# Kernel tuning notes

Measured on AMD Instinct MI355X. Metric: run time of the kernel, lower is better.

The kernel has to match this reference:

```python
import jax, jax.numpy as jnp
import numpy as np

B, T, D, TY = 64, 512, 96, 512
H, DK = 4, 32            # num_heads, embed_dim_per_head
E = H * DK               # embed_dim = 128
P = 2                    # function='L' -> 2 coefficients
L, HID = 64, 128         # latent_dim, hidden_dim


def setup_inputs() -> dict:
    key = jax.random.key(0)
    ks = jax.random.split(key, 16)
    inp = {
        "timesteps": jax.random.uniform(ks[0], (B, T), jnp.float32),
        "X": jax.random.normal(ks[1], (B, T, D), jnp.float32),
        "M": jax.random.randint(ks[2], (B, T, D), 0, 2).astype(jnp.float32),
        "y_time_steps": jax.random.uniform(ks[3], (B, TY), jnp.float32),
        # time_embedding: Linear(1, E)
        "te_w": jax.random.normal(ks[4], (E,), jnp.float32),
        "te_b": jax.random.normal(ks[5], (E,), jnp.float32) * 0.1,
        # learned query [1, P, E]
        "query": jax.random.normal(ks[6], (1, P, E), jnp.float32),
        # query_map / key_map: Linear(E, E), stored [in, out]
        "q_w": jax.random.normal(ks[7], (E, E), jnp.float32) / np.sqrt(E),
        "q_b": jax.random.normal(ks[8], (E,), jnp.float32) * 0.1,
        "k_w": jax.random.normal(ks[9], (E, E), jnp.float32) / np.sqrt(E),
        "k_b": jax.random.normal(ks[10], (E,), jnp.float32) * 0.1,
        # attn shared out: Linear(2D*H, L)
        "ow": jax.random.normal(ks[11], (2 * D * H, L), jnp.float32) / np.sqrt(2 * D * H),
        "ob": jnp.zeros((L,), jnp.float32),
        # decoder MLP: Linear(L,HID)+ReLU+Linear(HID,D)
        "w1": jax.random.normal(ks[12], (L, HID), jnp.float32) / np.sqrt(L),
        "b1": jnp.zeros((HID,), jnp.float32),
        "w2": jax.random.normal(ks[13], (HID, D), jnp.float32) / np.sqrt(HID),
        "b2": jnp.zeros((D,), jnp.float32),
    }
    return inp


def _fld_forward(timesteps, X, M, y_time_steps, te_w, te_b, query,
                 q_w, q_b, k_w, k_b, ow, ob, w1, b1, w2, b2):
    b, t, d = X.shape
    # time embedding: Linear(1,E), sin applied to indices i % H == 0
    emb = timesteps[..., None] * te_w + te_b               # [B,T,E]
    sin_idx = (jnp.arange(E) % H) == 0
    emb = jnp.where(sin_idx, jnp.sin(emb), emb)

    X_cat = jnp.concatenate([X, M], axis=-1)               # [B,T,2D]
    M_cat = jnp.concatenate([M, M], axis=-1)               # [B,T,2D]

    q = query @ q_w + q_b                                   # [1,P,E]
    k = emb @ k_w + k_b                                     # [B,T,E]
    q = q.reshape(1, P, H, DK).transpose(0, 2, 1, 3)        # [1,H,P,dk]
    k = k.reshape(b, t, H, DK).transpose(0, 2, 1, 3)        # [B,H,T,dk]

    scores = jnp.einsum('xhpd,bhtd->bhpt', q, k) / np.sqrt(DK)  # [B,H,P,T]
    # broadcast over value feature dim, mask per-feature, softmax over T
    logits = jnp.where(M_cat[:, None, None, :, :] == 0, -jnp.inf,
                       scores[..., None])                   # [B,H,P,T,2D]
    p = jax.nn.softmax(logits, axis=-2)
    xa = jnp.einsum('bhptf,btf->bhpf', p, X_cat)            # [B,H,P,2D]
    xa = xa.transpose(0, 2, 1, 3).reshape(b, P, H * 2 * d)  # [B,P,H*2D]
    coeffs = xa @ ow + ob                                   # [B,P,L]

    # function 'L': linear in y_time_steps
    x = coeffs[:, 0][:, None, :] + y_time_steps[:, :, None] * coeffs[:, 1][:, None, :]
    h1 = jax.nn.relu(x @ w1 + b1)
    return h1 @ w2 + b2                                     # [B,TY,D]


def reference(timesteps, X, M, y_time_steps, te_w, te_b, query,
              q_w, q_b, k_w, k_b, ow, ob, w1, b1, w2, b2):
    return _fld_forward(timesteps, X, M, y_time_steps, te_w, te_b, query,
                        q_w, q_b, k_w, k_b, ow, ob, w1, b1, w2, b2)
```

## Files before the change

kernel.cpp:

```cpp
#include <hip/hip_runtime.h>
#include <math.h>

#define B_   64
#define T_   512
#define D_   96
#define TY_  512
#define H_   4
#define DK_  32
#define E_   128
#define P_   2
#define L_   64
#define HID_ 128

#define WS_OB2P  1024
#define WS_PN    2048
#define WS_PD    395264

__global__ __launch_bounds__(256) void kspool(
    const float* __restrict__ tsteps, const float* __restrict__ te_w,
    const float* __restrict__ te_b,   const float* __restrict__ X,
    const float* __restrict__ M,      const float* __restrict__ query,
    const float* __restrict__ q_w,    const float* __restrict__ q_b,
    const float* __restrict__ k_w,    const float* __restrict__ k_b,
    const float* __restrict__ ow,     float* __restrict__ ws)
{
    const int c = blockIdx.x, b = blockIdx.y, tid = threadIdx.x;
    __shared__ float qm[P_ * E_];
    __shared__ float w2q_s[E_ * 8];
    __shared__ float tw_s[E_], tb_s[E_], bq_s[8];
    __shared__ float w_s[64 * 8];
    __shared__ float red[96 * 17];
    __shared__ float obp2[4][64];

    {
        int p = tid >> 7, ep = tid & 127;
        float acc = q_b[ep];
        #pragma unroll 4
        for (int e = 0; e < E_; ++e)
            acc += query[p * E_ + e] * q_w[e * E_ + ep];
        qm[p * E_ + ep] = acc;
    }
    if (tid < E_) { tw_s[tid] = te_w[tid]; tb_s[tid] = te_b[tid]; }
    __syncthreads();
    const float rs = 0.17677669529663687f;
    #pragma unroll
    for (int i = 0; i < 4; ++i) {
        int idx = tid + i * 256;
        int e = idx >> 3, hp = idx & 7, h = hp >> 1, p = hp & 1;
        float acc = 0.f;
        #pragma unroll
        for (int dk = 0; dk < DK_; ++dk)
            acc += k_w[e * E_ + h * DK_ + dk] * qm[p * E_ + h * DK_ + dk];
        w2q_s[idx] = acc * rs;
    }
    if (tid < 8) {
        int hp = tid, h = hp >> 1, p = hp & 1;
        float acc = 0.f;
        #pragma unroll
        for (int dk = 0; dk < DK_; ++dk)
            acc += k_b[h * DK_ + dk] * qm[p * E_ + h * DK_ + dk];
        bq_s[hp] = acc * rs;
    }
    __syncthreads();

    {
        const int t = tid & 63, hpg = tid >> 6, hp0 = hpg * 2;
        const float tv = tsteps[b * T_ + c * 64 + t];
        float a0 = 0.f, a1 = 0.f;
        #pragma unroll 4
        for (int e = 0; e < E_; ++e) {
            float v = tv * tw_s[e] + tb_s[e];
            if ((e & 3) == 0) v = __sinf(v);
            float2 w = *(const float2*)&w2q_s[e * 8 + hp0];
            a0 += v * w.x;
            a1 += v * w.y;
        }
        w_s[t * 8 + hp0]     = __expf(a0 + bq_s[hp0]);
        w_s[t * 8 + hp0 + 1] = __expf(a1 + bq_s[hp0 + 1]);
    }
    __syncthreads();

    const int fid = tid & 127, slice = tid >> 7;
    float num[8] = {0.f, 0.f, 0.f, 0.f, 0.f, 0.f, 0.f, 0.f};
    float den[8] = {0.f, 0.f, 0.f, 0.f, 0.f, 0.f, 0.f, 0.f};
    if (fid < 96) {
        #pragma unroll 4
        for (int i = 0; i < 32; ++i) {
            int tl = slice + 2 * i;
            size_t base = ((size_t)(b * T_ + c * 64 + tl)) * D_ + fid;
            float m = M[base], x = X[base];
            float mx = m * x;
            const float* wr = w_s + tl * 8;
            #pragma unroll
            for (int hp = 0; hp < 8; ++hp) {
                num[hp] += wr[hp] * mx;
                den[hp] += wr[hp] * m;
            }
        }
    }
    __syncthreads();
    if (slice == 1 && fid < 96) {
        #pragma unroll
        for (int hp = 0; hp < 8; ++hp) {
            red[fid * 17 + hp]     = num[hp];
            red[fid * 17 + 8 + hp] = den[hp];
        }
    }
    __syncthreads();
    if (slice == 0 && fid < 96) {
        float* pN = ws + WS_PN + ((size_t)((b * 8 + c) * 8)) * 96;
        float* pD = ws + WS_PD + ((size_t)((b * 8 + c) * 8)) * 96;
        #pragma unroll
        for (int hp = 0; hp < 8; ++hp) {
            pN[hp * 96 + fid] = num[hp] + red[fid * 17 + hp];
            pD[hp * 96 + fid] = den[hp] + red[fid * 17 + 8 + hp];
        }
    }

    if (b == 0) {
        int sub = tid >> 6, l = tid & 63;
        float acc = 0.f;
        #pragma unroll
        for (int k = 0; k < 12; ++k) {
            int hj = c * 48 + sub * 12 + k;
            int h = hj / 96, j = hj - h * 96;
            acc += ow[(size_t)(h * 2 * D_ + D_ + j) * L_ + l];
        }
        obp2[sub][l] = acc;
        __syncthreads();
        if (sub == 0)
            ws[WS_OB2P + c * 64 + l] = obp2[0][l] + obp2[1][l] + obp2[2][l] + obp2[3][l];
    }
}

__global__ __launch_bounds__(256) void kdecf(
    const float* __restrict__ yts, const float* __restrict__ ow,
    const float* __restrict__ w1,  const float* __restrict__ b1,
    const float* __restrict__ ob,  const float* __restrict__ w2,
    const float* __restrict__ b2,  const float* __restrict__ ws,
    float* __restrict__ out)
{
    __shared__ float xa_s[8 * 96];
    __shared__ float cfp[4][2][64];
    __shared__ float cf_s[2][64];
    __shared__ float abp[2][2][128];
    __shared__ float a0_s[HID_], a1_s[HID_];
    __shared__ float y_s[64];
    __shared__ float h_s[HID_ * 64];
    const int tid = threadIdx.x;
    const int bx = blockIdx.x;
    const int b = bx >> 3;
    const int posb = bx * 64;

    if (tid < 64) y_s[tid] = yts[posb + tid];

    for (int flat = tid; flat < 8 * 96; flat += 256) {
        int hp = flat / 96, f = flat - hp * 96;
        float n = 0.f, d = 0.f;
        #pragma unroll
        for (int c = 0; c < 8; ++c) {
            n += ws[WS_PN + ((size_t)((b * 8 + c) * 8 + hp)) * 96 + f];
            d += ws[WS_PD + ((size_t)((b * 8 + c) * 8 + hp)) * 96 + f];
        }
        xa_s[flat] = n / d;
    }
    __syncthreads();

    #pragma unroll
    for (int it = 0; it < 2; ++it) {
        int idx = tid + it * 256;
        int h = idx >> 7, p = (idx >> 6) & 1, l = idx & 63;
        const float* xr = xa_s + (h * 2 + p) * 96;
        const float* owr = ow + (size_t)(h * 2 * D_) * L_ + l;
        float acc = 0.f;
        #pragma unroll 4
        for (int f = 0; f < 96; ++f)
            acc += xr[f] * owr[(size_t)f * L_];
        cfp[h][p][l] = acc;
    }
    __syncthreads();

    if (tid < 128) {
        int p = tid >> 6, l = tid & 63;
        float v = cfp[0][p][l] + cfp[1][p][l] + cfp[2][p][l] + cfp[3][p][l] + ob[l];
        #pragma unroll
        for (int g = 0; g < 8; ++g) v += ws[WS_OB2P + g * 64 + l];
        cf_s[p][l] = v;
    }
    __syncthreads();

    {
        int s = tid >> 7, j = tid & 127;
        float a0 = 0.f, a1 = 0.f;
        #pragma unroll 4
        for (int li = 0; li < 32; ++li) {
            int l = s * 32 + li;
            float wv = w1[l * HID_ + j];
            a0 += cf_s[0][l] * wv;
            a1 += cf_s[1][l] * wv;
        }
        abp[s][0][j] = a0;
        abp[s][1][j] = a1;
    }
    __syncthreads();

    if (tid < 128) {
        a0_s[tid] = abp[0][0][tid] + abp[1][0][tid] + b1[tid];
    } else {
        int j = tid - 128;
        a1_s[j] = abp[0][1][j] + abp[1][1][j];
    }
    __syncthreads();

    #pragma unroll 4
    for (int r = 0; r < 32; ++r) {
        int flat = r * 256 + tid;
        int j = flat >> 6, pos = flat & 63;
        h_s[flat] = fmaxf(0.f, a0_s[j] + y_s[pos] * a1_s[j]);
    }
    __syncthreads();

    const int pg = tid >> 4, dg = tid & 15;
    const int p0 = pg * 4, d0 = dg * 6;
    float acc[4][6];
    #pragma unroll
    for (int pp = 0; pp < 4; ++pp)
        #pragma unroll
        for (int dd = 0; dd < 6; ++dd) acc[pp][dd] = 0.f;

    #pragma unroll 2
    for (int j = 0; j < HID_; ++j) {
        float4 h4 = *(const float4*)&h_s[j * 64 + p0];
        const float* wr = w2 + j * D_ + d0;
        float wv[6];
        #pragma unroll
        for (int dd = 0; dd < 6; ++dd) wv[dd] = wr[dd];
        const float hv[4] = {h4.x, h4.y, h4.z, h4.w};
        #pragma unroll
        for (int pp = 0; pp < 4; ++pp)
            #pragma unroll
            for (int dd = 0; dd < 6; ++dd)
                acc[pp][dd] += hv[pp] * wv[dd];
    }

    float bv[6];
    #pragma unroll
    for (int dd = 0; dd < 6; ++dd) bv[dd] = b2[d0 + dd];
    #pragma unroll
    for (int pp = 0; pp < 4; ++pp) {
        size_t obase = ((size_t)(posb + p0 + pp)) * D_ + d0;
        #pragma unroll
        for (int dd = 0; dd < 6; ++dd) out[obase + dd] = acc[pp][dd] + bv[dd];
    }
}

extern "C" void kernel_launch(void* const* d_in, const int* in_sizes, int n_in,
                              void* d_out, int out_size, void* d_ws, size_t ws_size,
                              hipStream_t stream)
{
    const float* timesteps = (const float*)d_in[0];
    const float* X         = (const float*)d_in[1];
    const float* M         = (const float*)d_in[2];
    const float* yts       = (const float*)d_in[3];
    const float* te_w      = (const float*)d_in[4];
    const float* te_b      = (const float*)d_in[5];
    const float* query     = (const float*)d_in[6];
    const float* q_w       = (const float*)d_in[7];
    const float* q_b       = (const float*)d_in[8];
    const float* k_w       = (const float*)d_in[9];
    const float* k_b       = (const float*)d_in[10];
    const float* ow        = (const float*)d_in[11];
    const float* ob        = (const float*)d_in[12];
    const float* w1        = (const float*)d_in[13];
    const float* b1        = (const float*)d_in[14];
    const float* w2        = (const float*)d_in[15];
    const float* b2        = (const float*)d_in[16];
    float* out = (float*)d_out;
    float* ws  = (float*)d_ws;

    kspool<<<dim3(8, B_), 256, 0, stream>>>(timesteps, te_w, te_b, X, M,
                                            query, q_w, q_b, k_w, k_b, ow, ws);
    kdecf<<<(B_ * TY_) / 64, 256, 0, stream>>>(yts, ow, w1, b1, ob, w2, b2, ws, out);
}
```

Measured before the change: 168.5 us.

## Split per-batch coefficient computation from decoder and stage w2 in LDS

The old decoder kernel redid the per-batch reduction and coefficient/first-layer projection in each of its 512 blocks. That work now runs once per batch in a separate 64-block kernel, which writes the a0/a1 vectors to workspace. The decoder loads w2 into shared memory, computes the hidden activation on the fly per thread (no h_s buffer), and writes output with float4 stores. The cost is an extra kernel launch and a 48KB LDS footprint per block, which may limit occupancy.

```diff
diff --git a/kernel.cpp b/kernel.cpp
--- a/kernel.cpp
+++ b/kernel.cpp
@@ -15,6 +15,7 @@
 #define WS_OB2P  1024
 #define WS_PN    2048
 #define WS_PD    395264
+#define WS_AB    788480
 
 __global__ __launch_bounds__(256) void kspool(
     const float* __restrict__ tsteps, const float* __restrict__ te_w,
@@ -133,26 +134,16 @@
     }
 }
 
-__global__ __launch_bounds__(256) void kdecf(
-    const float* __restrict__ yts, const float* __restrict__ ow,
-    const float* __restrict__ w1,  const float* __restrict__ b1,
-    const float* __restrict__ ob,  const float* __restrict__ w2,
-    const float* __restrict__ b2,  const float* __restrict__ ws,
-    float* __restrict__ out)
-{
+__global__ __launch_bounds__(256) void kab(
+    const float* __restrict__ ow, const float* __restrict__ w1,
+    const float* __restrict__ b1, const float* __restrict__ ob,
+    float* __restrict__ ws)
+{
+    const int b = blockIdx.x, tid = threadIdx.x;
     __shared__ float xa_s[8 * 96];
     __shared__ float cfp[4][2][64];
     __shared__ float cf_s[2][64];
     __shared__ float abp[2][2][128];
-    __shared__ float a0_s[HID_], a1_s[HID_];
-    __shared__ float y_s[64];
-    __shared__ float h_s[HID_ * 64];
-    const int tid = threadIdx.x;
-    const int bx = blockIdx.x;
-    const int b = bx >> 3;
-    const int posb = bx * 64;
-
-    if (tid < 64) y_s[tid] = yts[posb + tid];
 
     for (int flat = tid; flat < 8 * 96; flat += 256) {
         int hp = flat / 96, f = flat - hp * 96;
@@ -205,52 +196,71 @@
     __syncthreads();
 
     if (tid < 128) {
-        a0_s[tid] = abp[0][0][tid] + abp[1][0][tid] + b1[tid];
+        ws[WS_AB + b * 256 + tid] = abp[0][0][tid] + abp[1][0][tid] + b1[tid];
     } else {
         int j = tid - 128;
-        a1_s[j] = abp[0][1][j] + abp[1][1][j];
-    }
-    __syncthreads();
+        ws[WS_AB + b * 256 + 128 + j] = abp[0][1][j] + abp[1][1][j];
+    }
+}
+
+__global__ __launch_bounds__(256) void kdec(
+    const float* __restrict__ yts, const float* __restrict__ w2,
+    const float* __restrict__ b2,  const float* __restrict__ ws,
+    float* __restrict__ out)
+{
+    __shared__ float w2_s[HID_ * D_];
+    __shared__ float a0_s[HID_], a1_s[HID_];
+    __shared__ float y_s[64];
+    const int tid = threadIdx.x;
+    const int posb = blockIdx.x * 64;
+    const int b = posb >> 9;
+
+    {
+        const float4* src = (const float4*)w2;
+        float4* dst = (float4*)w2_s;
+        #pragma unroll
+        for (int i = 0; i < 12; ++i) dst[tid + i * 256] = src[tid + i * 256];
+    }
+    if (tid < 64) y_s[tid] = yts[posb + tid];
+    if (tid >= 64 && tid < 192) {
+        int j = tid - 64;
+        a0_s[j] = ws[WS_AB + b * 256 + j];
+        a1_s[j] = ws[WS_AB + b * 256 + 128 + j];
+    }
+    __syncthreads();
+
+    const int pos = tid & 63, ds = tid >> 6;
+    const float y = y_s[pos];
+    const float* wrow = w2_s + ds * 24;
+
+    float acc[24];
+    #pragma unroll
+    for (int dd = 0; dd < 24; ++dd) acc[dd] = 0.f;
 
     #pragma unroll 4
-    for (int r = 0; r < 32; ++r) {
-        int flat = r * 256 + tid;
-        int j = flat >> 6, pos = flat & 63;
-        h_s[flat] = fmaxf(0.f, a0_s[j] + y_s[pos] * a1_s[j]);
-    }
-    __syncthreads();
-
-    const int pg = tid >> 4, dg = tid & 15;
-    const int p0 = pg * 4, d0 = dg * 6;
-    float acc[4][6];
-    #pragma unroll
-    for (int pp = 0; pp < 4; ++pp)
-        #pragma unroll
-        for (int dd = 0; dd < 6; ++dd) acc[pp][dd] = 0.f;
-
-    #pragma unroll 2
     for (int j = 0; j < HID_; ++j) {
-        float4 h4 = *(const float4*)&h_s[j * 64 + p0];
-        const float* wr = w2 + j * D_ + d0;
-        float wv[6];
-        #pragma unroll
-        for (int dd = 0; dd < 6; ++dd) wv[dd] = wr[dd];
-        const float hv[4] = {h4.x, h4.y, h4.z, h4.w};
-        #pragma unroll
-        for (int pp = 0; pp < 4; ++pp)
-            #pragma unroll
-            for (int dd = 0; dd < 6; ++dd)
-                acc[pp][dd] += hv[pp] * wv[dd];
-    }
-
-    float bv[6];
-    #pragma unroll
-    for (int dd = 0; dd < 6; ++dd) bv[dd] = b2[d0 + dd];
-    #pragma unroll
-    for (int pp = 0; pp < 4; ++pp) {
-        size_t obase = ((size_t)(posb + p0 + pp)) * D_ + d0;
-        #pragma unroll
-        for (int dd = 0; dd < 6; ++dd) out[obase + dd] = acc[pp][dd] + bv[dd];
+        float h = fmaxf(0.f, a0_s[j] + y * a1_s[j]);
+        const float* wr = wrow + j * D_;
+        #pragma unroll
+        for (int q = 0; q < 6; ++q) {
+            float4 w4 = *(const float4*)(wr + q * 4);
+            acc[q * 4 + 0] += h * w4.x;
+            acc[q * 4 + 1] += h * w4.y;
+            acc[q * 4 + 2] += h * w4.z;
+            acc[q * 4 + 3] += h * w4.w;
+        }
+    }
+
+    float* op = out + ((size_t)(posb + pos)) * D_ + ds * 24;
+    const float* bp = b2 + ds * 24;
+    #pragma unroll
+    for (int q = 0; q < 6; ++q) {
+        float4 v;
+        v.x = acc[q * 4 + 0] + bp[q * 4 + 0];
+        v.y = acc[q * 4 + 1] + bp[q * 4 + 1];
+        v.z = acc[q * 4 + 2] + bp[q * 4 + 2];
+        v.w = acc[q * 4 + 3] + bp[q * 4 + 3];
+        *(float4*)(op + q * 4) = v;
     }
 }
 
@@ -280,5 +290,6 @@
 
     kspool<<<dim3(8, B_), 256, 0, stream>>>(timesteps, te_w, te_b, X, M,
                                             query, q_w, q_b, k_w, k_b, ow, ws);
-    kdecf<<<(B_ * TY_) / 64, 256, 0, stream>>>(yts, ow, w1, b1, ob, w2, b2, ws, out);
-}
+    kab<<<B_, 256, 0, stream>>>(ow, w1, b1, ob, ws);
+    kdec<<<(B_ * TY_) / 64, 256, 0, stream>>>(yts, w2, b2, ws, out);
+}
```

Result: faster. 163.2 us (median of 2 runs) (-3.2%).
